# Kernel tuning notes

Hardware: AMD Instinct MI355X
Metric: run time of the kernel (lower is better)

The kernel has to match this reference:

```python
import jax, jax.numpy as jnp
import numpy as np

B, S, D, H = 2, 2048, 1024, 16
HD = D // H  # head_dim = 64
SCALE = HD ** -0.5


def setup_inputs() -> dict:
    key = jax.random.key(0)
    ks = jax.random.split(key, 5)
    s = 0.02
    return {
        "query": jax.random.normal(ks[0], (B, S, D), dtype=jnp.float32),
        "Wq": jax.random.normal(ks[1], (D, D), dtype=jnp.float32) * s,
        "bq": jnp.zeros((D,), dtype=jnp.float32),
        "Wk": jax.random.normal(ks[2], (D, D), dtype=jnp.float32) * s,
        "bk": jnp.zeros((D,), dtype=jnp.float32),
        "Wv": jax.random.normal(ks[3], (D, D), dtype=jnp.float32) * s,
        "bv": jnp.zeros((D,), dtype=jnp.float32),
        "Wo": jax.random.normal(ks[4], (D, D), dtype=jnp.float32) * s,
        "bo": jnp.zeros((D,), dtype=jnp.float32),
    }


def reference(query, Wq, bq, Wk, bk, Wv, bv, Wo, bo):
    b, s, _ = query.shape
    # QKV projections (self-attention: key = value = query)
    Q = (query @ Wq + bq).reshape(b, s, H, HD).transpose(0, 2, 1, 3)  # bhqd
    K = (query @ Wk + bk).reshape(b, s, H, HD).transpose(0, 2, 1, 3)  # bhkd
    V = (query @ Wv + bv).reshape(b, s, H, HD).transpose(0, 2, 1, 3)  # bhvd
    scores = jnp.einsum('bhqd,bhkd->bhqk', Q, K) * SCALE
    weights = jax.nn.softmax(scores, axis=-1)
    out = jnp.einsum('bhqk,bhkd->bhqd', weights, V)
    out = out.transpose(0, 2, 1, 3).reshape(b, s, D)
    return out @ Wo + bo
```

## Files before the change

### kernel.cpp

```cpp
#include <hip/hip_runtime.h>
#include <hip/hip_bf16.h>
#include <math.h>

#define B_ 2
#define S_ 2048
#define D_ 1024
#define H_ 16
#define HD_ 64
#define M_ (B_*S_)
#define C1_ 0.1803368798f

typedef float f32x4 __attribute__((ext_vector_type(4)));
typedef float f32x16 __attribute__((ext_vector_type(16)));
typedef short s16x8 __attribute__((ext_vector_type(8)));

__device__ __forceinline__ short f2bf(float f) {
  union { float f; unsigned u; } x; x.f = f;
  unsigned r = x.u + 0x7fffu + ((x.u >> 16) & 1u);
  return (short)(r >> 16);
}
__device__ __forceinline__ float bf2f(short v) {
  union { unsigned u; float f; } x; x.u = ((unsigned)(unsigned short)v) << 16;
  return x.f;
}
__device__ __forceinline__ unsigned cvt_pk_bf16(float a, float b) {
  unsigned r;
  asm("v_cvt_pk_bf16_f32 %0, %1, %2" : "=v"(r) : "v"(a), "v"(b));
  return r;
}
__device__ __forceinline__ float exp2_fast(float x) {
#if __has_builtin(__builtin_amdgcn_exp2f)
  return __builtin_amdgcn_exp2f(x);
#else
  float r; asm("v_exp_f32 %0, %1" : "=v"(r) : "v"(x)); return r;
#endif
}
__device__ __forceinline__ void gload_lds16(const void* g, void* l) {
  __builtin_amdgcn_global_load_lds(
      (const __attribute__((address_space(1))) void*)g,
      (__attribute__((address_space(3))) void*)l, 16, 0, 0);
}

__global__ __launch_bounds__(256) void k_prep(
    const float* __restrict__ query, short* __restrict__ xbf,
    const float* __restrict__ W0, const float* __restrict__ W1,
    const float* __restrict__ W2, const float* __restrict__ W3,
    short* __restrict__ T0, short* __restrict__ T1,
    short* __restrict__ T2, short* __restrict__ T3) {
  __shared__ short lt[64][72];
  const int blk = blockIdx.x;
  const int t = threadIdx.x;
  if (blk < 1024) {
    const int z = blk >> 8, tile = blk & 255;
    const float* W = z == 0 ? W0 : z == 1 ? W1 : z == 2 ? W2 : W3;
    short* Wt      = z == 0 ? T0 : z == 1 ? T1 : z == 2 ? T2 : T3;
    const int r0 = (tile >> 4) * 64;
    const int c0 = (tile & 15) * 64;
    const int rr = t >> 4, c4 = (t & 15) * 4;
    #pragma unroll
    for (int p = 0; p < 4; ++p) {
      int row = p * 16 + rr;
      f32x4 v = *reinterpret_cast<const f32x4*>(W + (size_t)(r0 + row) * D_ + c0 + c4);
      #pragma unroll
      for (int j = 0; j < 4; ++j) lt[c4 + j][row] = f2bf(v[j]);
    }
    __syncthreads();
    #pragma unroll
    for (int p = 0; p < 2; ++p) {
      int slot = p * 256 + t;
      int row = slot >> 3, s = slot & 7;
      s16x8 v = *reinterpret_cast<const s16x8*>(&lt[row][s * 8]);
      *reinterpret_cast<s16x8*>(Wt + (size_t)(c0 + row) * D_ + r0 + s * 8) = v;
    }
  } else {
    int i = ((blk - 1024) * 256 + t) * 8;
    f32x4 a = *reinterpret_cast<const f32x4*>(query + i);
    f32x4 b = *reinterpret_cast<const f32x4*>(query + i + 4);
    s16x8 v;
    v[0]=f2bf(a[0]); v[1]=f2bf(a[1]); v[2]=f2bf(a[2]); v[3]=f2bf(a[3]);
    v[4]=f2bf(b[0]); v[5]=f2bf(b[1]); v[6]=f2bf(b[2]); v[7]=f2bf(b[3]);
    *reinterpret_cast<s16x8*>(xbf + i) = v;
  }
}

__global__ __launch_bounds__(256) void k_gemm_qkv(
    const short* __restrict__ A,
    const short* __restrict__ WtQ, const short* __restrict__ WtK, const short* __restrict__ WtV,
    const float* __restrict__ bQ, const float* __restrict__ bK, const float* __restrict__ bV,
    short* __restrict__ Qo, short* __restrict__ Ko, short* __restrict__ Vto) {
  __shared__ __align__(16) char lds[65536];
  const int z = blockIdx.z;
  const short* Bt   = z == 0 ? WtQ : z == 1 ? WtK : WtV;
  const float* bias = z == 0 ? bQ  : z == 1 ? bK  : bV;
  const int t = threadIdx.x;
  const int lane = t & 63, wid = t >> 6;
  const int l15 = lane & 15, l4 = lane >> 4;
  const int wm = wid >> 1, wn = wid & 1;
  const int m0 = blockIdx.x * 128, n0 = blockIdx.y * 128;

  f32x4 acc[4][4];
  #pragma unroll
  for (int i = 0; i < 4; ++i)
    #pragma unroll
    for (int j = 0; j < 4; ++j) acc[i][j] = (f32x4){0.f, 0.f, 0.f, 0.f};

  auto stage = [&](int k0, int buf) {
    char* base = lds + buf * 32768;
    #pragma unroll
    for (int i = 0; i < 4; ++i) {
      int slot = t + i * 256;
      int row = slot >> 3, sw = (t & 7) ^ (row & 7);
      gload_lds16(A  + (size_t)(m0 + row) * D_ + k0 + sw * 8, base + (i * 256 + wid * 64) * 16);
      gload_lds16(Bt + (size_t)(n0 + row) * D_ + k0 + sw * 8, base + 16384 + (i * 256 + wid * 64) * 16);
    }
  };

  stage(0, 0);
  __syncthreads();

  int buf = 0;
  for (int k0 = 0; k0 < D_; k0 += 64, buf ^= 1) {
    if (k0 + 64 < D_) stage(k0 + 64, buf ^ 1);
    const char* bA = lds + buf * 32768;
    const char* bB = bA + 16384;
    #pragma unroll
    for (int ks = 0; ks < 2; ++ks) {
      s16x8 af[4], bf[4];
      #pragma unroll
      for (int mt = 0; mt < 4; ++mt) {
        int row = wm * 64 + mt * 16 + l15;
        af[mt] = *reinterpret_cast<const s16x8*>(bA + row * 128 + (((ks*4 + l4) ^ (row & 7)) * 16));
      }
      #pragma unroll
      for (int nt = 0; nt < 4; ++nt) {
        int row = wn * 64 + nt * 16 + l15;
        bf[nt] = *reinterpret_cast<const s16x8*>(bB + row * 128 + (((ks*4 + l4) ^ (row & 7)) * 16));
      }
      #pragma unroll
      for (int mt = 0; mt < 4; ++mt)
        #pragma unroll
        for (int nt = 0; nt < 4; ++nt)
          acc[mt][nt] = __builtin_amdgcn_mfma_f32_16x16x32_bf16(af[mt], bf[nt], acc[mt][nt], 0, 0, 0);
    }
    __syncthreads();
  }

  const float scale = (z == 0) ? C1_ : 1.f;
  #pragma unroll
  for (int nt = 0; nt < 4; ++nt) {
    int cl = wn * 64 + nt * 16 + l15;
    float bv = bias[n0 + cl];
    #pragma unroll
    for (int mt = 0; mt < 4; ++mt) {
      #pragma unroll
      for (int r = 0; r < 4; ++r) {
        int rl = wm * 64 + mt * 16 + l4 * 4 + r;
        short hv = f2bf((acc[mt][nt][r] + bv) * scale);
        if (z == 2) *reinterpret_cast<short*>(lds + cl * 256 + rl * 2) = hv;
        else        *reinterpret_cast<short*>(lds + rl * 256 + cl * 2) = hv;
      }
    }
  }
  __syncthreads();
  short* outp = (z == 0) ? Qo : (z == 1) ? Ko : Vto;
  const size_t ld   = (z == 2) ? (size_t)M_ : (size_t)D_;
  const int rowbase = (z == 2) ? n0 : m0;
  const int colbase = (z == 2) ? m0 : n0;
  #pragma unroll
  for (int p = 0; p < 8; ++p) {
    int slot = p * 256 + t;
    int row = slot >> 4, s = slot & 15;
    s16x8 v = *reinterpret_cast<const s16x8*>(lds + row * 256 + s * 16);
    *reinterpret_cast<s16x8*>(outp + (size_t)(rowbase + row) * ld + colbase + s * 8) = v;
  }
}

__global__ __launch_bounds__(256) void k_gemm_out(const short* __restrict__ A,
                                                  const short* __restrict__ Bt,
                                                  const float* __restrict__ bias,
                                                  float* __restrict__ C) {
  __shared__ __align__(16) char lds[49152];
  const int t = threadIdx.x;
  const int lane = t & 63, wid = t >> 6;
  const int l15 = lane & 15, l4 = lane >> 4;
  const int wm = wid >> 1, wn = wid & 1;
  const int m0 = blockIdx.x * 128, n0 = blockIdx.y * 64;

  f32x4 acc[4][2];
  #pragma unroll
  for (int i = 0; i < 4; ++i)
    #pragma unroll
    for (int j = 0; j < 2; ++j) acc[i][j] = (f32x4){0.f, 0.f, 0.f, 0.f};

  auto stage = [&](int k0, int buf) {
    char* base = lds + buf * 24576;
    #pragma unroll
    for (int i = 0; i < 4; ++i) {
      int slot = t + i * 256;
      int row = slot >> 3, sw = (t & 7) ^ (row & 7);
      gload_lds16(A + (size_t)(m0 + row) * D_ + k0 + sw * 8, base + (i * 256 + wid * 64) * 16);
    }
    #pragma unroll
    for (int i = 0; i < 2; ++i) {
      int slot = t + i * 256;
      int row = slot >> 3, sw = (t & 7) ^ (row & 7);
      gload_lds16(Bt + (size_t)(n0 + row) * D_ + k0 + sw * 8,
                  base + 16384 + (i * 256 + wid * 64) * 16);
    }
  };

  stage(0, 0);
  __syncthreads();

  int buf = 0;
  for (int k0 = 0; k0 < D_; k0 += 64, buf ^= 1) {
    if (k0 + 64 < D_) stage(k0 + 64, buf ^ 1);
    const char* bA = lds + buf * 24576;
    const char* bB = bA + 16384;
    #pragma unroll
    for (int ks = 0; ks < 2; ++ks) {
      s16x8 af[4], bf[2];
      #pragma unroll
      for (int mt = 0; mt < 4; ++mt) {
        int row = wm * 64 + mt * 16 + l15;
        af[mt] = *reinterpret_cast<const s16x8*>(bA + row * 128 + (((ks*4 + l4) ^ (row & 7)) * 16));
      }
      #pragma unroll
      for (int nt = 0; nt < 2; ++nt) {
        int row = wn * 32 + nt * 16 + l15;
        bf[nt] = *reinterpret_cast<const s16x8*>(bB + row * 128 + (((ks*4 + l4) ^ (row & 7)) * 16));
      }
      #pragma unroll
      for (int mt = 0; mt < 4; ++mt)
        #pragma unroll
        for (int nt = 0; nt < 2; ++nt)
          acc[mt][nt] = __builtin_amdgcn_mfma_f32_16x16x32_bf16(af[mt], bf[nt], acc[mt][nt], 0, 0, 0);
    }
    __syncthreads();
  }
  #pragma unroll
  for (int nt = 0; nt < 2; ++nt) {
    int col = n0 + wn * 32 + nt * 16 + l15;
    float bv = bias[col];
    #pragma unroll
    for (int mt = 0; mt < 4; ++mt) {
      int row0 = m0 + wm * 64 + mt * 16 + l4 * 4;
      #pragma unroll
      for (int r = 0; r < 4; ++r)
        C[(size_t)(row0 + r) * D_ + col] = acc[mt][nt][r] + bv;
    }
  }
}

__global__ __launch_bounds__(256, 2) void k_attn(const short* __restrict__ Q,
                                                 const short* __restrict__ K,
                                                 const short* __restrict__ Vt,
                                                 short* __restrict__ U0,
                                                 short* __restrict__ U1,
                                                 float* __restrict__ lsum) {
  __shared__ __align__(16) char lds[32768];
  const int t = threadIdx.x;
  const int lane = t & 63, wid = t >> 6;
  const int l31 = lane & 31, hi = lane >> 5;
  const int orig = blockIdx.x;
  const int xcd = orig & 7, idx = orig >> 3;
  const int bh = xcd * 4 + (idx >> 4);
  const int rem = idx & 15;
  const int qblk = rem >> 1;
  const int half = rem & 1;
  const int b = bh >> 4, h = bh & 15;
  const int q0 = qblk * 256;
  const size_t qkbase = (size_t)b * S_ * D_ + h * HD_;
  const short* gK = K + qkbase + (size_t)(half * (S_ / 2)) * D_;
  const short* gVt = Vt + (size_t)(h * HD_) * M_ + (size_t)b * S_ + half * (S_ / 2);
  short* Up = half ? U1 : U0;

  s16x8 qfA[4], qfB[4];
  {
    const short* qa = Q + qkbase + (size_t)(q0 + wid * 64 + l31) * D_ + hi * 8;
    const short* qb = qa + (size_t)32 * D_;
    #pragma unroll
    for (int ks = 0; ks < 4; ++ks) {
      qfA[ks] = *reinterpret_cast<const s16x8*>(qa + ks * 16);
      qfB[ks] = *reinterpret_cast<const s16x8*>(qb + ks * 16);
    }
  }

  f32x16 oaA[2], oaB[2];
  #pragma unroll
  for (int i = 0; i < 16; ++i) { oaA[0][i] = 0.f; oaA[1][i] = 0.f; oaB[0][i] = 0.f; oaB[1][i] = 0.f; }
  float lA = 0.f, lB = 0.f;

  const int tr3 = t >> 3;
  const int ssw8 = ((t & 7) ^ (tr3 & 7)) * 8;
  const size_t kSrc = (size_t)tr3 * D_ + ssw8;
  const size_t vSrc = (size_t)tr3 * M_ + ssw8;

  const int s7 = l31 & 7;
  const int rbase = l31 * 128;
  int soff[4];
  #pragma unroll
  for (int ks = 0; ks < 4; ++ks) soff[ks] = ((2 * ks + hi) ^ s7) * 16;

  auto stage = [&](int tl, int bb) {
    if (tl >= S_ / 128) return;
    const short* pk = gK + (size_t)(tl * 64) * D_ + kSrc;
    const short* pv = gVt + tl * 64 + vSrc;
    char* dK = lds + bb * 8192 + wid * 1024;
    char* dV = dK + 16384;
    gload_lds16(pk, dK);
    gload_lds16(pk + (size_t)32 * D_, dK + 4096);
    gload_lds16(pv, dV);
    gload_lds16(pv + (size_t)32 * M_, dV + 4096);
  };

  auto tileFn = [&](int bb, int tl) {
    stage(tl + 1, bb ^ 1);
    const char* bK = lds + bb * 8192;
    const char* bV = bK + 16384;

    f32x16 scA[2], scB[2];
    #pragma unroll
    for (int i = 0; i < 16; ++i) { scA[0][i] = 0.f; scA[1][i] = 0.f; scB[0][i] = 0.f; scB[1][i] = 0.f; }
    __builtin_amdgcn_s_setprio(1);
    #pragma unroll
    for (int ks = 0; ks < 4; ++ks)
      #pragma unroll
      for (int blk = 0; blk < 2; ++blk) {
        s16x8 kf = *reinterpret_cast<const s16x8*>(bK + blk * 4096 + rbase + soff[ks]);
        scA[blk] = __builtin_amdgcn_mfma_f32_32x32x16_bf16(kf, qfA[ks], scA[blk], 0, 0, 0);
        scB[blk] = __builtin_amdgcn_mfma_f32_32x32x16_bf16(kf, qfB[ks], scB[blk], 0, 0, 0);
      }
    __builtin_amdgcn_s_setprio(0);

    float rsA = 0.f, rsB = 0.f;
    unsigned pA1[2][4], pA2[2][4], pB1[2][4], pB2[2][4];
    #pragma unroll
    for (int blk = 0; blk < 2; ++blk)
      #pragma unroll
      for (int g = 0; g < 4; ++g) {
        float a0 = exp2_fast(scA[blk][4*g+0]), a1 = exp2_fast(scA[blk][4*g+1]);
        float a2 = exp2_fast(scA[blk][4*g+2]), a3 = exp2_fast(scA[blk][4*g+3]);
        rsA += (a0 + a1) + (a2 + a3);
        pA1[blk][g] = cvt_pk_bf16(a0, a1);
        pA2[blk][g] = cvt_pk_bf16(a2, a3);
        float b0 = exp2_fast(scB[blk][4*g+0]), b1 = exp2_fast(scB[blk][4*g+1]);
        float b2 = exp2_fast(scB[blk][4*g+2]), b3 = exp2_fast(scB[blk][4*g+3]);
        rsB += (b0 + b1) + (b2 + b3);
        pB1[blk][g] = cvt_pk_bf16(b0, b1);
        pB2[blk][g] = cvt_pk_bf16(b2, b3);
      }
    rsA += __shfl_xor(rsA, 32);
    rsB += __shfl_xor(rsB, 32);
    lA += rsA;
    lB += rsB;

    __builtin_amdgcn_s_setprio(1);
    #pragma unroll
    for (int sp = 0; sp < 4; ++sp) {
      const int blk = sp >> 1, su = sp & 1;
      unsigned xa0 = pA1[blk][2*su],     xa1 = pA2[blk][2*su];
      unsigned xb0 = pA1[blk][2*su + 1], xb1 = pA2[blk][2*su + 1];
      asm("v_permlane32_swap_b32 %0, %1" : "+v"(xa0), "+v"(xb0));
      asm("v_permlane32_swap_b32 %0, %1" : "+v"(xa1), "+v"(xb1));
      union { unsigned u[4]; s16x8 v; } pwA;
      pwA.u[0] = xa0; pwA.u[1] = xa1; pwA.u[2] = xb0; pwA.u[3] = xb1;
      unsigned ya0 = pB1[blk][2*su],     ya1 = pB2[blk][2*su];
      unsigned yb0 = pB1[blk][2*su + 1], yb1 = pB2[blk][2*su + 1];
      asm("v_permlane32_swap_b32 %0, %1" : "+v"(ya0), "+v"(yb0));
      asm("v_permlane32_swap_b32 %0, %1" : "+v"(ya1), "+v"(yb1));
      union { unsigned u[4]; s16x8 v; } pwB;
      pwB.u[0] = ya0; pwB.u[1] = ya1; pwB.u[2] = yb0; pwB.u[3] = yb1;
      #pragma unroll
      for (int dblk = 0; dblk < 2; ++dblk) {
        s16x8 vf = *reinterpret_cast<const s16x8*>(bV + dblk * 4096 + rbase + soff[sp]);
        oaA[dblk] = __builtin_amdgcn_mfma_f32_32x32x16_bf16(pwA.v, vf, oaA[dblk], 0, 0, 0);
        oaB[dblk] = __builtin_amdgcn_mfma_f32_32x32x16_bf16(pwB.v, vf, oaB[dblk], 0, 0, 0);
      }
    }
    __builtin_amdgcn_s_setprio(0);
    __syncthreads();
  };

  stage(0, 0);
  __syncthreads();
  #pragma unroll 1
  for (int it = 0; it < S_ / 256; ++it) {
    tileFn(0, 2 * it);
    tileFn(1, 2 * it + 1);
  }

  char* myl = lds + wid * 8192;
  #pragma unroll
  for (int reg = 0; reg < 16; ++reg) {
    int qrow = (reg & 3) + 8 * (reg >> 2) + 4 * hi;
    *reinterpret_cast<short*>(myl + qrow * 128 + l31 * 2)              = f2bf(oaA[0][reg]);
    *reinterpret_cast<short*>(myl + qrow * 128 + (32 + l31) * 2)       = f2bf(oaA[1][reg]);
    *reinterpret_cast<short*>(myl + (32 + qrow) * 128 + l31 * 2)       = f2bf(oaB[0][reg]);
    *reinterpret_cast<short*>(myl + (32 + qrow) * 128 + (32 + l31) * 2) = f2bf(oaB[1][reg]);
  }
  #pragma unroll
  for (int i = 0; i < 8; ++i) {
    int slot = i * 64 + lane;
    int row = slot >> 3, s = slot & 7;
    s16x8 v = *reinterpret_cast<const s16x8*>(myl + slot * 16);
    *reinterpret_cast<s16x8*>(
        Up + qkbase + (size_t)(q0 + wid * 64 + row) * D_ + s * 8) = v;
  }
  if (hi == 0) {
    int qb = ((half * 32 + bh) << 11) + q0 + wid * 64 + l31;
    lsum[qb] = lA;
    lsum[qb + 32] = lB;
  }
}

__global__ __launch_bounds__(256) void k_merge(const short* U0, const short* U1,
                                               const float* lsum, short* out) {
  int i = (blockIdx.x * 256 + threadIdx.x) * 8;
  int row = i >> 10;
  int col = i & 1023;
  int b = row >> 11, s = row & 2047;
  int bh = b * 16 + (col >> 6);
  float l0 = lsum[(bh << 11) + s];
  float l1 = lsum[((32 + bh) << 11) + s];
  float inv = 1.f / (l0 + l1);
  s16x8 u0 = *reinterpret_cast<const s16x8*>(U0 + i);
  s16x8 u1 = *reinterpret_cast<const s16x8*>(U1 + i);
  s16x8 r;
  #pragma unroll
  for (int j = 0; j < 8; ++j) r[j] = f2bf((bf2f(u0[j]) + bf2f(u1[j])) * inv);
  *reinterpret_cast<s16x8*>(out + i) = r;
}

extern "C" void kernel_launch(void* const* d_in, const int* in_sizes, int n_in,
                              void* d_out, int out_size, void* d_ws, size_t ws_size,
                              hipStream_t stream) {
  const float* query = (const float*)d_in[0];
  const float* Wq = (const float*)d_in[1];
  const float* bq = (const float*)d_in[2];
  const float* Wk = (const float*)d_in[3];
  const float* bk = (const float*)d_in[4];
  const float* Wv = (const float*)d_in[5];
  const float* bv = (const float*)d_in[6];
  const float* Wo = (const float*)d_in[7];
  const float* bo = (const float*)d_in[8];
  float* out = (float*)d_out;

  const size_t NE = (size_t)M_ * D_;
  short* ws   = (short*)d_ws;
  short* xbf  = ws;
  short* qbf  = ws + NE;
  short* kbf  = ws + 2 * NE;
  short* vtbf = ws + 3 * NE;
  short* aout = ws + 4 * NE;
  short* wtq  = ws + 5 * NE;
  short* wtk  = wtq + (size_t)D_ * D_;
  short* wtv  = wtk + (size_t)D_ * D_;
  short* wto  = wtv + (size_t)D_ * D_;

  short* U0 = aout;
  short* U1 = xbf;
  float* lsb = (float*)wtq;

  k_prep<<<3072, 256, 0, stream>>>(query, xbf, Wq, Wk, Wv, Wo, wtq, wtk, wtv, wto);

  k_gemm_qkv<<<dim3(M_ / 128, D_ / 128, 3), 256, 0, stream>>>(
      xbf, wtq, wtk, wtv, bq, bk, bv, qbf, kbf, vtbf);

  k_attn<<<512, 256, 0, stream>>>(qbf, kbf, vtbf, U0, U1, lsb);
  k_merge<<<(int)(NE / (8 * 256)), 256, 0, stream>>>(U0, U1, lsb, aout);

  k_gemm_out<<<dim3(M_ / 128, D_ / 64), 256, 0, stream>>>(aout, wto, bo, out);
}
```

Measured before the change: 100.6 us.

## Fuse split-KV merge normalization into output projection GEMM A-tile loading

Removes the separate k_merge kernel. The output GEMM now loads both partial attention outputs into registers, combines them with the row-sum reciprocal, and writes the merged bf16 A tile to LDS, replacing the direct global-to-LDS copy. This saves one launch and the write and re-read of the merged buffer. In exchange, the GEMM loads twice as much A data per tile, spends more registers on the prefetch, and repeats the merge for every N-block (16 times).

```diff
diff --git a/kernel.cpp b/kernel.cpp
--- a/kernel.cpp
+++ b/kernel.cpp
@@ -175,7 +175,9 @@
   }
 }
 
-__global__ __launch_bounds__(256) void k_gemm_out(const short* __restrict__ A,
+__global__ __launch_bounds__(256) void k_gemm_out(const short* __restrict__ U0,
+                                                  const short* __restrict__ U1,
+                                                  const float* __restrict__ lsum,
                                                   const short* __restrict__ Bt,
                                                   const float* __restrict__ bias,
                                                   float* __restrict__ C) {
@@ -186,35 +188,66 @@
   const int wm = wid >> 1, wn = wid & 1;
   const int m0 = blockIdx.x * 128, n0 = blockIdx.y * 64;
 
+  int arow[4]; size_t aoff[4]; int asl[4]; int lrow[4];
+  #pragma unroll
+  for (int i = 0; i < 4; ++i) {
+    int slot = t + i * 256;
+    int row = slot >> 3, sw = (t & 7) ^ (row & 7);
+    arow[i] = row;
+    aoff[i] = (size_t)(m0 + row) * D_ + sw * 8;
+    asl[i] = slot * 16;
+    int gr = m0 + row;
+    lrow[i] = ((gr >> 11) * 16 << 11) + (gr & 2047);
+  }
+
   f32x4 acc[4][2];
   #pragma unroll
   for (int i = 0; i < 4; ++i)
     #pragma unroll
     for (int j = 0; j < 2; ++j) acc[i][j] = (f32x4){0.f, 0.f, 0.f, 0.f};
 
-  auto stage = [&](int k0, int buf) {
+  s16x8 u0v[4], u1v[4];
+  auto loadA = [&](int k0) {
+    #pragma unroll
+    for (int i = 0; i < 4; ++i) {
+      u0v[i] = *reinterpret_cast<const s16x8*>(U0 + aoff[i] + k0);
+      u1v[i] = *reinterpret_cast<const s16x8*>(U1 + aoff[i] + k0);
+    }
+  };
+  auto writeA = [&](int k0, int buf) {
+    const int hsh = (k0 >> 6) << 11;
     char* base = lds + buf * 24576;
     #pragma unroll
     for (int i = 0; i < 4; ++i) {
-      int slot = t + i * 256;
-      int row = slot >> 3, sw = (t & 7) ^ (row & 7);
-      gload_lds16(A + (size_t)(m0 + row) * D_ + k0 + sw * 8, base + (i * 256 + wid * 64) * 16);
-    }
+      float l0 = lsum[lrow[i] + hsh];
+      float l1 = lsum[lrow[i] + hsh + (32 << 11)];
+      float inv = 1.f / (l0 + l1);
+      s16x8 m;
+      #pragma unroll
+      for (int j = 0; j < 8; ++j)
+        m[j] = f2bf((bf2f(u0v[i][j]) + bf2f(u1v[i][j])) * inv);
+      *reinterpret_cast<s16x8*>(base + asl[i]) = m;
+    }
+  };
+  auto stageB = [&](int k0, int buf) {
+    char* base = lds + buf * 24576 + 16384;
     #pragma unroll
     for (int i = 0; i < 2; ++i) {
       int slot = t + i * 256;
       int row = slot >> 3, sw = (t & 7) ^ (row & 7);
       gload_lds16(Bt + (size_t)(n0 + row) * D_ + k0 + sw * 8,
-                  base + 16384 + (i * 256 + wid * 64) * 16);
-    }
-  };
-
-  stage(0, 0);
+                  base + (i * 256 + wid * 64) * 16);
+    }
+  };
+
+  loadA(0);
+  stageB(0, 0);
+  writeA(0, 0);
   __syncthreads();
 
   int buf = 0;
   for (int k0 = 0; k0 < D_; k0 += 64, buf ^= 1) {
-    if (k0 + 64 < D_) stage(k0 + 64, buf ^ 1);
+    if (k0 + 64 < D_) { loadA(k0 + 64); stageB(k0 + 64, buf ^ 1); }
     const char* bA = lds + buf * 24576;
     const char* bB = bA + 16384;
     #pragma unroll
@@ -236,6 +269,7 @@
         for (int nt = 0; nt < 2; ++nt)
           acc[mt][nt] = __builtin_amdgcn_mfma_f32_16x16x32_bf16(af[mt], bf[nt], acc[mt][nt], 0, 0, 0);
     }
+    if (k0 + 64 < D_) writeA(k0 + 64, buf ^ 1);
     __syncthreads();
   }
   #pragma unroll
@@ -394,9 +428,9 @@
   #pragma unroll
   for (int reg = 0; reg < 16; ++reg) {
     int qrow = (reg & 3) + 8 * (reg >> 2) + 4 * hi;
-    *reinterpret_cast<short*>(myl + qrow * 128 + l31 * 2)              = f2bf(oaA[0][reg]);
-    *reinterpret_cast<short*>(myl + qrow * 128 + (32 + l31) * 2)       = f2bf(oaA[1][reg]);
-    *reinterpret_cast<short*>(myl + (32 + qrow) * 128 + l31 * 2)       = f2bf(oaB[0][reg]);
+    *reinterpret_cast<short*>(myl + qrow * 128 + l31 * 2)               = f2bf(oaA[0][reg]);
+    *reinterpret_cast<short*>(myl + qrow * 128 + (32 + l31) * 2)        = f2bf(oaA[1][reg]);
+    *reinterpret_cast<short*>(myl + (32 + qrow) * 128 + l31 * 2)        = f2bf(oaB[0][reg]);
     *reinterpret_cast<short*>(myl + (32 + qrow) * 128 + (32 + l31) * 2) = f2bf(oaB[1][reg]);
   }
   #pragma unroll
@@ -412,24 +446,6 @@
     lsum[qb] = lA;
     lsum[qb + 32] = lB;
   }
-}
-
-__global__ __launch_bounds__(256) void k_merge(const short* U0, const short* U1,
-                                               const float* lsum, short* out) {
-  int i = (blockIdx.x * 256 + threadIdx.x) * 8;
-  int row = i >> 10;
-  int col = i & 1023;
-  int b = row >> 11, s = row & 2047;
-  int bh = b * 16 + (col >> 6);
-  float l0 = lsum[(bh << 11) + s];
-  float l1 = lsum[((32 + bh) << 11) + s];
-  float inv = 1.f / (l0 + l1);
-  s16x8 u0 = *reinterpret_cast<const s16x8*>(U0 + i);
-  s16x8 u1 = *reinterpret_cast<const s16x8*>(U1 + i);
-  s16x8 r;
-  #pragma unroll
-  for (int j = 0; j < 8; ++j) r[j] = f2bf((bf2f(u0[j]) + bf2f(u1[j])) * inv);
-  *reinterpret_cast<s16x8*>(out + i) = r;
 }
 
 extern "C" void kernel_launch(void* const* d_in, const int* in_sizes, int n_in,
@@ -452,13 +468,13 @@
   short* qbf  = ws + NE;
   short* kbf  = ws + 2 * NE;
   short* vtbf = ws + 3 * NE;
-  short* aout = ws + 4 * NE;
+  short* u0b  = ws + 4 * NE;
   short* wtq  = ws + 5 * NE;
   short* wtk  = wtq + (size_t)D_ * D_;
   short* wtv  = wtk + (size_t)D_ * D_;
   short* wto  = wtv + (size_t)D_ * D_;
 
-  short* U0 = aout;
+  short* U0 = u0b;
   short* U1 = xbf;
   float* lsb = (float*)wtq;
 
@@ -468,7 +484,6 @@
       xbf, wtq, wtk, wtv, bq, bk, bv, qbf, kbf, vtbf);
 
   k_attn<<<512, 256, 0, stream>>>(qbf, kbf, vtbf, U0, U1, lsb);
-  k_merge<<<(int)(NE / (8 * 256)), 256, 0, stream>>>(U0, U1, lsb, aout);
-
-  k_gemm_out<<<dim3(M_ / 128, D_ / 64), 256, 0, stream>>>(aout, wto, bo, out);
-}
+
+  k_gemm_out<<<dim3(M_ / 128, D_ / 64), 256, 0, stream>>>(U0, U1, lsb, wto, bo, out);
+}
```

New measurement: 122.7 us. 1.22x slower.
